# Performance work log

Hardware: AMD Instinct MI355X
Metric: run time of the kernel (lower is better)

## Reference

```python
import jax, jax.numpy as jnp
import numpy as np

QMAX = 7.0  # 4-bit symmetric: levels in [-8, 7]

def quant4(w):
    # per-tensor symmetric 4-bit fake-quant with straight-through estimator
    s = jnp.max(jnp.abs(w)) / QMAX
    q = jnp.clip(jnp.round(w / s), -8.0, 7.0) * s
    return w + jax.lax.stop_gradient(q - w)

def setup_inputs() -> dict:
    key = jax.random.key(0)
    ks = jax.random.split(key, 7)
    B = 2048
    x = jax.random.normal(ks[0], (B, 1, 31, 16, 31), dtype=jnp.float32)
    # conv: out_ch=1, in_ch=1, kernel (5,3,5)
    w_conv = jax.random.normal(ks[1], (1, 1, 5, 3, 5), dtype=jnp.float32) * 0.1
    b_conv = jax.random.normal(ks[2], (1,), dtype=jnp.float32) * 0.1
    w_fc1 = jax.random.normal(ks[3], (128, 343), dtype=jnp.float32) * 0.05
    b_fc1 = jax.random.normal(ks[4], (128,), dtype=jnp.float32) * 0.05
    w_fc2 = jax.random.normal(ks[5], (4, 128), dtype=jnp.float32) * 0.05
    b_fc2 = jax.random.normal(ks[6], (4,), dtype=jnp.float32) * 0.05
    return {"x": x, "w_conv": w_conv, "b_conv": b_conv,
            "w_fc1": w_fc1, "b_fc1": b_fc1, "w_fc2": w_fc2, "b_fc2": b_fc2}

def reference(x, w_conv, b_conv, w_fc1, b_fc1, w_fc2, b_fc2):
    # QuantConv3d: 4-bit quantized weights, stride (2,1,2), no padding
    c1 = jax.lax.conv_general_dilated(
        x, quant4(w_conv), window_strides=(2, 1, 2), padding='VALID',
        dimension_numbers=('NCDHW', 'OIDHW', 'NCDHW'))
    c1 = c1 + b_conv.reshape(1, -1, 1, 1, 1)          # [B,1,14,14,14]
    # MaxPool3d(2)
    p1 = jax.lax.reduce_window(c1, -jnp.inf, jax.lax.max,
                               (1, 1, 2, 2, 2), (1, 1, 2, 2, 2), 'VALID')  # [B,1,7,7,7]
    f = p1.reshape(p1.shape[0], -1)                   # [B,343]
    a1 = jax.nn.relu(f @ quant4(w_fc1).T + b_fc1)     # [B,128]
    s2 = a1 @ quant4(w_fc2).T + b_fc2                 # [B,4]
    return jax.nn.softmax(s2, axis=1)
```

## Files before the change

kernel.cpp:

```cpp
#include <hip/hip_runtime.h>
#include <hip/hip_bf16.h>

#define WS_WCONV   128
#define WS_W1T     256
#define WS_W2      44160
#define WS_FEAT    45056

__device__ __forceinline__ float q4(float w, float s) {
  if (s <= 0.f) return 0.f;
  float r = rintf(w / s);
  r = fminf(fmaxf(r, -8.f), 7.f);
  return r * s;
}

__global__ __launch_bounds__(256) void quant_all(
    const float* __restrict__ wconv, const float* __restrict__ w1,
    const float* __restrict__ w2, float* __restrict__ ws) {
  __shared__ float red[256];
  int b = blockIdx.x, t = threadIdx.x;
  if (b < 88) {
    const float4* w4 = (const float4*)w1;
    float m = 0.f;
    for (int i = t; i < 10976; i += 256) {
      float4 v = w4[i];
      m = fmaxf(m, fmaxf(fmaxf(fabsf(v.x), fabsf(v.y)),
                         fmaxf(fabsf(v.z), fabsf(v.w))));
    }
    red[t] = m;
    __syncthreads();
    for (int s = 128; s > 0; s >>= 1) {
      if (t < s) red[t] = fmaxf(red[t], red[t + s]);
      __syncthreads();
    }
    float s = red[0] * (1.0f / 7.0f);
    #pragma unroll
    for (int k = 0; k < 2; ++k) {
      int idx = b * 512 + k * 256 + t;
      if (idx < 43904) {
        float q = q4(w1[idx], s);
        int o = idx / 343;
        int j = idx - o * 343;
        ws[WS_W1T + j * 128 + o] = q;
      }
    }
  } else {
    float mc = (t < 75) ? fabsf(wconv[t]) : 0.f;
    float m2 = 0.f;
    for (int i = t; i < 512; i += 256) m2 = fmaxf(m2, fabsf(w2[i]));
    red[t] = mc;
    __syncthreads();
    for (int s = 128; s > 0; s >>= 1) {
      if (t < s) red[t] = fmaxf(red[t], red[t + s]);
      __syncthreads();
    }
    float sc = red[0] * (1.0f / 7.0f);
    __syncthreads();
    red[t] = m2;
    __syncthreads();
    for (int s = 128; s > 0; s >>= 1) {
      if (t < s) red[t] = fmaxf(red[t], red[t + s]);
      __syncthreads();
    }
    float s2 = red[0] * (1.0f / 7.0f);
    if (t < 75) ws[WS_WCONV + t] = q4(wconv[t], sc);
    #pragma unroll
    for (int k = 0; k < 2; ++k) {
      int idx = k * 256 + t;
      ws[WS_W2 + idx] = q4(w2[idx], s2);
    }
  }
}

__global__ __launch_bounds__(256, 4) void conv_pool(
    const float* __restrict__ x, const float* __restrict__ bconv,
    const float* __restrict__ ws, float* __restrict__ feat) {
  __shared__ float xs[9424];
  int t = threadIdx.x;
  int half = blockIdx.x & 1;
  int b = blockIdx.x >> 1;
  int d0 = half ? 16 : 0;
  int nfl4 = half ? 1860 : 2356;

  const float4* src = (const float4*)(x + (size_t)b * 15376 + d0 * 496);
  float4* dst = (float4*)xs;
  for (int i = t; i < nfl4; i += 256) dst[i] = src[i];
  __syncthreads();

  int npf = half ? 147 : 196;
  if (t < npf) {
    int pdl = t / 49;
    int rr  = t - pdl * 49;
    int ph  = rr / 7;
    int pw  = rr - ph * 7;
    const float* wq = ws + WS_WCONV;
    float c[2][2][2];
    #pragma unroll
    for (int i = 0; i < 8; ++i) ((float*)c)[i] = 0.f;

    int base0 = pdl * (4 * 496) + ph * 62 + pw * 4;
    #pragma unroll
    for (int dd = 0; dd < 7; ++dd) {
      int rbase = base0 + dd * 496;
      #pragma unroll
      for (int hh = 0; hh < 4; ++hh) {
        float row[7];
        #pragma unroll
        for (int wi = 0; wi < 7; ++wi) row[wi] = xs[rbase + hh * 31 + wi];
        #pragma unroll
        for (int odp = 0; odp < 2; ++odp) {
          int kd = dd - 2 * odp;
          if (kd < 0 || kd > 4) continue;
          #pragma unroll
          for (int ohp = 0; ohp < 2; ++ohp) {
            int kh = hh - ohp;
            if (kh < 0 || kh > 2) continue;
            #pragma unroll
            for (int owp = 0; owp < 2; ++owp) {
              float a = c[odp][ohp][owp];
              #pragma unroll
              for (int kw = 0; kw < 5; ++kw)
                a = fmaf(row[2 * owp + kw], wq[kd * 15 + kh * 5 + kw], a);
              c[odp][ohp][owp] = a;
            }
          }
        }
      }
    }
    float m = ((float*)c)[0];
    #pragma unroll
    for (int i = 1; i < 8; ++i) m = fmaxf(m, ((float*)c)[i]);
    int pd = pdl + (half ? 4 : 0);
    feat[b * 343 + pd * 49 + rr] = m + bconv[0];
  }
}

__global__ __launch_bounds__(256) void fc_head(
    const float* __restrict__ ws, const float* __restrict__ bfc1,
    const float* __restrict__ bfc2, float* __restrict__ out) {
  __shared__ float fs[2744];
  __shared__ float fc1p[8][128];
  __shared__ float a1s[8][132];
  __shared__ float s2[32];
  int t = threadIdx.x;
  int b0 = blockIdx.x * 8;

  const float4* fsrc = (const float4*)(ws + WS_FEAT + (size_t)b0 * 343);
  for (int i = t; i < 686; i += 256) ((float4*)fs)[i] = fsrc[i];
  __syncthreads();

  int g = t >> 7, o = t & 127;
  const float* w1T = ws + WS_W1T;
  float acc[8];
  #pragma unroll
  for (int i = 0; i < 8; ++i) acc[i] = 0.f;
  int j0 = g ? 172 : 0;
  int j1 = g ? 343 : 172;
  for (int j = j0; j < j1; ++j) {
    float w = w1T[j * 128 + o];
    #pragma unroll
    for (int bi = 0; bi < 8; ++bi)
      acc[bi] = fmaf(fs[bi * 343 + j], w, acc[bi]);
  }
  if (g) {
    #pragma unroll
    for (int bi = 0; bi < 8; ++bi) fc1p[bi][o] = acc[bi];
  }
  __syncthreads();
  if (!g) {
    float bo = bfc1[o];
    #pragma unroll
    for (int bi = 0; bi < 8; ++bi)
      a1s[bi][o] = fmaxf(acc[bi] + fc1p[bi][o] + bo, 0.f);
  }
  __syncthreads();
  if (t < 32) {
    int bb = t >> 2, cls = t & 3;
    const float* w2 = ws + WS_W2 + cls * 128;
    float a = bfc2[cls];
    for (int k = 0; k < 128; ++k) a = fmaf(a1s[bb][k], w2[k], a);
    s2[t] = a;
  }
  __syncthreads();
  if (t < 32) {
    int bb = t >> 2, cls = t & 3;
    float v0 = s2[bb * 4], v1 = s2[bb * 4 + 1];
    float v2 = s2[bb * 4 + 2], v3 = s2[bb * 4 + 3];
    float m = fmaxf(fmaxf(v0, v1), fmaxf(v2, v3));
    float e0 = expf(v0 - m), e1 = expf(v1 - m);
    float e2 = expf(v2 - m), e3 = expf(v3 - m);
    float inv = 1.f / (e0 + e1 + e2 + e3);
    float mine = (cls == 0) ? e0 : (cls == 1) ? e1 : (cls == 2) ? e2 : e3;
    out[(b0 + bb) * 4 + cls] = mine * inv;
  }
}

extern "C" void kernel_launch(void* const* d_in, const int* in_sizes, int n_in,
                              void* d_out, int out_size, void* d_ws, size_t ws_size,
                              hipStream_t stream) {
  const float* x     = (const float*)d_in[0];
  const float* wconv = (const float*)d_in[1];
  const float* bconv = (const float*)d_in[2];
  const float* wfc1  = (const float*)d_in[3];
  const float* bfc1  = (const float*)d_in[4];
  const float* wfc2  = (const float*)d_in[5];
  const float* bfc2  = (const float*)d_in[6];
  float* out = (float*)d_out;
  float* ws  = (float*)d_ws;

  quant_all<<<89, 256, 0, stream>>>(wconv, wfc1, wfc2, ws);
  conv_pool<<<4096, 256, 0, stream>>>(x, bconv, ws, ws + WS_FEAT);
  fc_head<<<256, 256, 0, stream>>>(ws, bfc1, bfc2, out);
}
```

Measured before the change: 266.0 us.

## Fuse conv-pool and FC head into one per-sample kernel

Merges the conv+maxpool kernel and the FC head into a single kernel, with one block per sample. Each block loads the input in two halves into LDS and keeps the pooled features in shared memory, so the feature buffer no longer round-trips through global memory and one launch is dropped. The trade-off is that every block rereads the full quantized fc1 weight matrix instead of sharing it across 8 samples, which multiplies L2 traffic. The two conv phases also run sequentially with partial thread utilization.

```diff
diff --git a/kernel.cpp b/kernel.cpp
--- a/kernel.cpp
+++ b/kernel.cpp
@@ -4,7 +4,6 @@
 #define WS_WCONV   128
 #define WS_W1T     256
 #define WS_W2      44160
-#define WS_FEAT    45056
 
 __device__ __forceinline__ float q4(float w, float s) {
   if (s <= 0.f) return 0.f;
@@ -71,126 +70,128 @@
   }
 }
 
-__global__ __launch_bounds__(256, 4) void conv_pool(
-    const float* __restrict__ x, const float* __restrict__ bconv,
-    const float* __restrict__ ws, float* __restrict__ feat) {
-  __shared__ float xs[9424];
-  int t = threadIdx.x;
-  int half = blockIdx.x & 1;
-  int b = blockIdx.x >> 1;
-  int d0 = half ? 16 : 0;
-  int nfl4 = half ? 1860 : 2356;
-
-  const float4* src = (const float4*)(x + (size_t)b * 15376 + d0 * 496);
-  float4* dst = (float4*)xs;
-  for (int i = t; i < nfl4; i += 256) dst[i] = src[i];
-  __syncthreads();
-
-  int npf = half ? 147 : 196;
-  if (t < npf) {
-    int pdl = t / 49;
-    int rr  = t - pdl * 49;
-    int ph  = rr / 7;
-    int pw  = rr - ph * 7;
-    const float* wq = ws + WS_WCONV;
-    float c[2][2][2];
-    #pragma unroll
-    for (int i = 0; i < 8; ++i) ((float*)c)[i] = 0.f;
-
-    int base0 = pdl * (4 * 496) + ph * 62 + pw * 4;
-    #pragma unroll
-    for (int dd = 0; dd < 7; ++dd) {
-      int rbase = base0 + dd * 496;
+__device__ __forceinline__ void conv_phase(
+    const float* __restrict__ xs, const float* __restrict__ wq,
+    int t, int npf, int pd_off, float bc, float* __restrict__ feat) {
+  if (t >= npf) return;
+  int pdl = t / 49;
+  int rr  = t - pdl * 49;
+  int ph  = rr / 7;
+  int pw  = rr - ph * 7;
+  float c[2][2][2];
+  #pragma unroll
+  for (int i = 0; i < 8; ++i) ((float*)c)[i] = 0.f;
+  int base0 = pdl * 1984 + ph * 62 + pw * 4;
+  #pragma unroll
+  for (int dd = 0; dd < 7; ++dd) {
+    int rbase = base0 + dd * 496;
+    #pragma unroll
+    for (int hh = 0; hh < 4; ++hh) {
+      float row[7];
       #pragma unroll
-      for (int hh = 0; hh < 4; ++hh) {
-        float row[7];
+      for (int wi = 0; wi < 7; ++wi) row[wi] = xs[rbase + hh * 31 + wi];
+      #pragma unroll
+      for (int odp = 0; odp < 2; ++odp) {
+        int kd = dd - 2 * odp;
+        if (kd < 0 || kd > 4) continue;
         #pragma unroll
-        for (int wi = 0; wi < 7; ++wi) row[wi] = xs[rbase + hh * 31 + wi];
-        #pragma unroll
-        for (int odp = 0; odp < 2; ++odp) {
-          int kd = dd - 2 * odp;
-          if (kd < 0 || kd > 4) continue;
+        for (int ohp = 0; ohp < 2; ++ohp) {
+          int kh = hh - ohp;
+          if (kh < 0 || kh > 2) continue;
           #pragma unroll
-          for (int ohp = 0; ohp < 2; ++ohp) {
-            int kh = hh - ohp;
-            if (kh < 0 || kh > 2) continue;
+          for (int owp = 0; owp < 2; ++owp) {
+            float a = c[odp][ohp][owp];
             #pragma unroll
-            for (int owp = 0; owp < 2; ++owp) {
-              float a = c[odp][ohp][owp];
-              #pragma unroll
-              for (int kw = 0; kw < 5; ++kw)
-                a = fmaf(row[2 * owp + kw], wq[kd * 15 + kh * 5 + kw], a);
-              c[odp][ohp][owp] = a;
-            }
+            for (int kw = 0; kw < 5; ++kw)
+              a = fmaf(row[2 * owp + kw], wq[kd * 15 + kh * 5 + kw], a);
+            c[odp][ohp][owp] = a;
           }
         }
       }
     }
-    float m = ((float*)c)[0];
-    #pragma unroll
-    for (int i = 1; i < 8; ++i) m = fmaxf(m, ((float*)c)[i]);
-    int pd = pdl + (half ? 4 : 0);
-    feat[b * 343 + pd * 49 + rr] = m + bconv[0];
-  }
-}
-
-__global__ __launch_bounds__(256) void fc_head(
+  }
+  float m = ((float*)c)[0];
+  #pragma unroll
+  for (int i = 1; i < 8; ++i) m = fmaxf(m, ((float*)c)[i]);
+  feat[(pdl + pd_off) * 49 + rr] = m + bc;
+}
+
+__global__ __launch_bounds__(256, 4) void fused_net(
+    const float* __restrict__ x, const float* __restrict__ bconv,
     const float* __restrict__ ws, const float* __restrict__ bfc1,
     const float* __restrict__ bfc2, float* __restrict__ out) {
-  __shared__ float fs[2744];
-  __shared__ float fc1p[8][128];
-  __shared__ float a1s[8][132];
-  __shared__ float s2[32];
+  __shared__ float xs[9424];
+  __shared__ float feat[344];
+  __shared__ float fc1p[128];
+  __shared__ float a1[128];
+  __shared__ float s2[4];
   int t = threadIdx.x;
-  int b0 = blockIdx.x * 8;
-
-  const float4* fsrc = (const float4*)(ws + WS_FEAT + (size_t)b0 * 343);
-  for (int i = t; i < 686; i += 256) ((float4*)fs)[i] = fsrc[i];
+  int b = blockIdx.x;
+  const float* wq = ws + WS_WCONV;
+  float bc = bconv[0];
+
+  {
+    const float4* src = (const float4*)(x + (size_t)b * 15376);
+    float4* dst = (float4*)xs;
+    for (int i = t; i < 2356; i += 256) dst[i] = src[i];
+    if (t == 0) feat[343] = 0.f;
+  }
+  __syncthreads();
+  conv_phase(xs, wq, t, 196, 0, bc, feat);
+  __syncthreads();
+  {
+    const float4* src = (const float4*)(x + (size_t)b * 15376 + 16 * 496);
+    float4* dst = (float4*)xs;
+    for (int i = t; i < 1860; i += 256) dst[i] = src[i];
+  }
+  __syncthreads();
+  conv_phase(xs, wq, t, 147, 4, bc, feat);
   __syncthreads();
 
   int g = t >> 7, o = t & 127;
-  const float* w1T = ws + WS_W1T;
-  float acc[8];
-  #pragma unroll
-  for (int i = 0; i < 8; ++i) acc[i] = 0.f;
-  int j0 = g ? 172 : 0;
-  int j1 = g ? 343 : 172;
-  for (int j = j0; j < j1; ++j) {
-    float w = w1T[j * 128 + o];
-    #pragma unroll
-    for (int bi = 0; bi < 8; ++bi)
-      acc[bi] = fmaf(fs[bi * 343 + j], w, acc[bi]);
-  }
-  if (g) {
-    #pragma unroll
-    for (int bi = 0; bi < 8; ++bi) fc1p[bi][o] = acc[bi];
-  }
-  __syncthreads();
-  if (!g) {
-    float bo = bfc1[o];
-    #pragma unroll
-    for (int bi = 0; bi < 8; ++bi)
-      a1s[bi][o] = fmaxf(acc[bi] + fc1p[bi][o] + bo, 0.f);
-  }
-  __syncthreads();
-  if (t < 32) {
-    int bb = t >> 2, cls = t & 3;
-    const float* w2 = ws + WS_W2 + cls * 128;
-    float a = bfc2[cls];
-    for (int k = 0; k < 128; ++k) a = fmaf(a1s[bb][k], w2[k], a);
-    s2[t] = a;
-  }
-  __syncthreads();
-  if (t < 32) {
-    int bb = t >> 2, cls = t & 3;
-    float v0 = s2[bb * 4], v1 = s2[bb * 4 + 1];
-    float v2 = s2[bb * 4 + 2], v3 = s2[bb * 4 + 3];
+  {
+    const float* w1T = ws + WS_W1T;
+    int j0 = g ? 172 : 0;
+    const float4* f4 = (const float4*)&feat[j0];
+    const float* wp = w1T + j0 * 128 + o;
+    float p0 = 0.f, p1 = 0.f, p2 = 0.f, p3 = 0.f;
+    for (int q = 0; q < 43; ++q) {
+      float4 ff = f4[q];
+      p0 = fmaf(ff.x, wp[0],   p0);
+      p1 = fmaf(ff.y, wp[128], p1);
+      p2 = fmaf(ff.z, wp[256], p2);
+      p3 = fmaf(ff.w, wp[384], p3);
+      wp += 512;
+    }
+    float acc = (p0 + p1) + (p2 + p3);
+    if (g) fc1p[o] = acc;
+    __syncthreads();
+    if (!g) a1[o] = fmaxf(acc + fc1p[o] + bfc1[o], 0.f);
+  }
+  __syncthreads();
+
+  if (t < 64) {
+    int cls = t & 3, kk = t >> 2;
+    const float* w2 = ws + WS_W2 + cls * 128 + kk * 8;
+    const float* av = a1 + kk * 8;
+    float p = 0.f;
+    #pragma unroll
+    for (int i = 0; i < 8; ++i) p = fmaf(av[i], w2[i], p);
+    p += __shfl_down(p, 32);
+    p += __shfl_down(p, 16);
+    p += __shfl_down(p, 8);
+    p += __shfl_down(p, 4);
+    if (t < 4) s2[t] = p + bfc2[t];
+  }
+  __syncthreads();
+  if (t < 4) {
+    float v0 = s2[0], v1 = s2[1], v2 = s2[2], v3 = s2[3];
     float m = fmaxf(fmaxf(v0, v1), fmaxf(v2, v3));
     float e0 = expf(v0 - m), e1 = expf(v1 - m);
     float e2 = expf(v2 - m), e3 = expf(v3 - m);
     float inv = 1.f / (e0 + e1 + e2 + e3);
-    float mine = (cls == 0) ? e0 : (cls == 1) ? e1 : (cls == 2) ? e2 : e3;
-    out[(b0 + bb) * 4 + cls] = mine * inv;
+    float mine = (t == 0) ? e0 : (t == 1) ? e1 : (t == 2) ? e2 : e3;
+    out[b * 4 + t] = mine * inv;
   }
 }
 
@@ -208,6 +209,5 @@
   float* ws  = (float*)d_ws;
 
   quant_all<<<89, 256, 0, stream>>>(wconv, wfc1, wfc2, ws);
-  conv_pool<<<4096, 256, 0, stream>>>(x, bconv, ws, ws + WS_FEAT);
-  fc_head<<<256, 256, 0, stream>>>(ws, bfc1, bfc2, out);
-}
+  fused_net<<<2048, 256, 0, stream>>>(x, bconv, ws, bfc1, bfc2, out);
+}
```

After: 225.7 us. 15.2% less time.
